# Performance work log

Hardware: AMD Instinct MI355X
Metric: run time of the kernel (lower is better)

The kernel has to match this reference:

```python
import jax, jax.numpy as jnp
import numpy as np

GAMMA = 0.99
ETA = 0.1
PHI = 0.9
EPS_FLOOR_NEWTON = 1e-8
EPS_FLOOR_BETA = 1e-6
N_NEWTON = 20


def _epsilon_cosh(r):
    # r: [B, N] nonnegative residuals; per-row Newton solve for epsilon s.t.
    # mean(sinh(r/eps)) == 1 along axis 1.
    N = r.shape[1]
    r_max = jnp.maximum(jnp.max(r, axis=1, keepdims=True), EPS_FLOOR_NEWTON)
    eps = r_max / (jnp.log(jnp.asarray(2.0 * N, dtype=r.dtype)) + EPS_FLOOR_NEWTON)
    for _ in range(N_NEWTON):
        eps_safe = jnp.maximum(eps, EPS_FLOOR_NEWTON)
        u = r / eps_safe  # [B, N]
        val = jnp.mean(jnp.sinh(u), axis=1, keepdims=True) - 1.0
        grad = jnp.mean(jnp.cosh(u) * (-u / eps_safe), axis=1, keepdims=True)
        eps = eps - val / (grad - EPS_FLOOR_NEWTON)
    return jnp.maximum(eps, EPS_FLOOR_NEWTON)


def _update_spatial_weights(r_i, Lambda, it):
    # 'cosh' weighting potential branch of update_spatial_weights
    del it  # unused by the cosh branch
    eps_q = _epsilon_cosh(r_i)                       # [B, 1]
    beta = 1.0 / (eps_q + EPS_FLOOR_BETA)            # [B, 1]
    q = jnp.sinh(beta * r_i)                         # [B, N]
    q_max = jnp.max(q, axis=1, keepdims=True)
    q_norm = q / (q_max + 1e-20)
    lambda_it = PHI * q_norm + (1.0 - PHI)
    return GAMMA * Lambda + ETA * lambda_it


def setup_inputs() -> dict:
    key = jax.random.key(0)
    k1, k2, k3 = jax.random.split(key, 3)
    B, N = 2048, 8192
    y_pred = jax.random.normal(k1, (B, N), dtype=jnp.float32)
    y_true = jax.random.normal(k2, (B, N), dtype=jnp.float32)
    Lambda = jax.random.uniform(k3, (B, N), dtype=jnp.float32)
    return {"y_pred": y_pred, "y_true": y_true, "Lambda": Lambda, "it": 100}


def reference(y_pred, y_true, Lambda, it):
    r_i = jnp.abs(y_true - y_pred)
    # weights are computed on detached residuals
    updated_Lambda = _update_spatial_weights(jax.lax.stop_gradient(r_i), Lambda, it)
    loss = jnp.mean(jnp.square(updated_Lambda * r_i))
    return (loss, updated_Lambda)
```

## Files before the change

### kernel.cpp

```cpp
#include <hip/hip_runtime.h>
#include <math.h>

#define N_COLS 8192
#define BLOCK  256
#define NW     4
#define F4PT   (N_COLS / BLOCK / 4)
#define NBINS  1024
#define BPL    (NBINS / 64)

__global__ void zero_out_kernel(float* out) {
    if (threadIdx.x == 0 && blockIdx.x == 0) out[0] = 0.0f;
}

__global__ __launch_bounds__(BLOCK) void custom_loss_kernel(
        const float* __restrict__ y_pred,
        const float* __restrict__ y_true,
        const float* __restrict__ Lambda,
        float* __restrict__ out,
        float inv_total) {
    __shared__ unsigned int s_hist[NBINS];
    __shared__ float s_wmax[NW];
    __shared__ float s_part[NW];
    __shared__ float s_bcast[2];

    const int row  = blockIdx.x;
    const int tid  = threadIdx.x;
    const int lane = tid & 63;
    const int wid  = tid >> 6;
    const size_t base = (size_t)row * N_COLS;
    const float4* yp4 = (const float4*)(y_pred + base);
    const float4* yt4 = (const float4*)(y_true + base);

    float4 r[F4PT];
    float rmax = 0.0f;
    #pragma unroll
    for (int j = 0; j < F4PT; ++j) {
        const int g = j * BLOCK + tid;
        float4 a = yt4[g];
        float4 b = yp4[g];
        float4 rv;
        rv.x = fabsf(a.x - b.x); rv.y = fabsf(a.y - b.y);
        rv.z = fabsf(a.z - b.z); rv.w = fabsf(a.w - b.w);
        r[j] = rv;
        rmax = fmaxf(rmax, fmaxf(fmaxf(rv.x, rv.y), fmaxf(rv.z, rv.w)));
    }
    #pragma unroll
    for (int m = 32; m >= 1; m >>= 1) rmax = fmaxf(rmax, __shfl_xor(rmax, m, 64));
    if (lane == 0) s_wmax[wid] = rmax;
    #pragma unroll
    for (int i = 0; i < NBINS / BLOCK; ++i) s_hist[tid + i * BLOCK] = 0u;
    __syncthreads();
    rmax = fmaxf(fmaxf(s_wmax[0], s_wmax[1]), fmaxf(s_wmax[2], s_wmax[3]));
    rmax = fmaxf(rmax, 1e-8f);

    const float hscale = (float)NBINS / rmax;
    #pragma unroll
    for (int j = 0; j < F4PT; ++j) {
        unsigned bx = min((unsigned)(r[j].x * hscale), (unsigned)(NBINS - 1));
        unsigned by = min((unsigned)(r[j].y * hscale), (unsigned)(NBINS - 1));
        unsigned bz = min((unsigned)(r[j].z * hscale), (unsigned)(NBINS - 1));
        unsigned bw = min((unsigned)(r[j].w * hscale), (unsigned)(NBINS - 1));
        atomicAdd(&s_hist[bx], 1u);
        atomicAdd(&s_hist[by], 1u);
        atomicAdd(&s_hist[bz], 1u);
        atomicAdd(&s_hist[bw], 1u);
    }
    __syncthreads();

    const float4* lam4 = (const float4*)(Lambda + base);
    float4 lam[F4PT];
    #pragma unroll
    for (int j = 0; j < F4PT; ++j) lam[j] = lam4[j * BLOCK + tid];

    if (wid == 0) {
        float eps = rmax / (logf(2.0f * (float)N_COLS) + 1e-8f);
        const float binw = rmax * (1.0f / (float)NBINS);
        const float sc2  = 0.5f / (float)N_COLS;
        for (int it = 0; it < 20; ++it) {
            const float inv_eps = __builtin_amdgcn_rcpf(fmaxf(eps, 1e-8f));
            const float d   = binw * inv_eps;
            const float d64 = 64.0f * d;
            float u  = ((float)lane + 0.5f) * d;
            float e  = __expf(u);
            float ei = __expf(-u);
            const float E  = __expf(d64);
            const float Ei = __expf(-d64);
            float fs = 0.0f, gs = 0.0f;
            #pragma unroll
            for (int k = 0; k < BPL; ++k) {
                const float n = (float)s_hist[lane + 64 * k];
                fs = fmaf(n, e - ei, fs);
                gs = fmaf(n * (e + ei), u, gs);
                e *= E; ei *= Ei; u += d64;
            }
            #pragma unroll
            for (int m2 = 32; m2 >= 1; m2 >>= 1) {
                fs += __shfl_xor(fs, m2, 64);
                gs += __shfl_xor(gs, m2, 64);
            }
            float val  = fmaf(fs, sc2, -1.0f);
            float grad = -(gs * sc2) * inv_eps;
            float delta = val * __builtin_amdgcn_rcpf(grad - 1e-8f);
            eps -= delta;
            if (fabsf(delta) <= 1e-5f * eps) break;
        }
        eps = fmaxf(eps, 1e-8f);
        const float beta = 1.0f / (eps + 1e-6f);
        const float um = beta * rmax;
        const float qmax = 0.5f * (__expf(um) - __expf(-um));
        if (lane == 0) {
            s_bcast[0] = beta;
            s_bcast[1] = 1.0f / (qmax + 1e-20f);
        }
    }
    __syncthreads();
    const float beta     = s_bcast[0];
    const float inv_qmax = s_bcast[1];

    float* outw = out + 1 + base;
    float s_loss = 0.0f;
    #pragma unroll
    for (int j = 0; j < F4PT; ++j) {
        const int g = j * BLOCK + tid;
        float rr[4] = {r[j].x, r[j].y, r[j].z, r[j].w};
        float LL[4] = {lam[j].x, lam[j].y, lam[j].z, lam[j].w};
        #pragma unroll
        for (int c = 0; c < 4; ++c) {
            float u  = beta * rr[c];
            float q  = 0.5f * (__expf(u) - __expf(-u));
            float lam_it = fmaf(0.9f, q * inv_qmax, 0.1f);
            float uL = fmaf(0.99f, LL[c], 0.1f * lam_it);
            outw[(size_t)g * 4 + c] = uL;
            float t = uL * rr[c];
            s_loss = fmaf(t, t, s_loss);
        }
    }
    #pragma unroll
    for (int m = 32; m >= 1; m >>= 1) s_loss += __shfl_xor(s_loss, m, 64);
    if (lane == 0) s_part[wid] = s_loss;
    __syncthreads();
    if (tid == 0) {
        float tot = (s_part[0] + s_part[1]) + (s_part[2] + s_part[3]);
        atomicAdd(out, tot * inv_total);
    }
}

extern "C" void kernel_launch(void* const* d_in, const int* in_sizes, int n_in,
                              void* d_out, int out_size, void* d_ws, size_t ws_size,
                              hipStream_t stream) {
    const float* y_pred = (const float*)d_in[0];
    const float* y_true = (const float*)d_in[1];
    const float* Lambda = (const float*)d_in[2];
    float* out = (float*)d_out;

    const int total = in_sizes[0];
    const int B = total / N_COLS;
    const float inv_total = 1.0f / (float)total;

    hipLaunchKernelGGL(zero_out_kernel, dim3(1), dim3(64), 0, stream, out);
    hipLaunchKernelGGL(custom_loss_kernel, dim3(B), dim3(BLOCK), 0, stream,
                       y_pred, y_true, Lambda, out, inv_total);
}
```

Baseline: 223.5 us.

## Split fused loss kernel into stats pass and epilogue pass

Splits the single per-row kernel into a stats kernel (max, histogram, Newton solve writing beta and inverse qmax to workspace) and an epilogue kernel that rereads y_pred and y_true, loads Lambda, and writes the updated weights and loss. The aim is to lower register pressure and raise occupancy, since the fused kernel kept residuals and Lambda in registers across the serial single-wave Newton loop. The cost is a second read of both inputs (about 134 MB extra traffic), which may partly come from L2/MALL, plus an extra kernel launch.

```diff
diff --git a/kernel.cpp b/kernel.cpp
--- a/kernel.cpp
+++ b/kernel.cpp
@@ -12,16 +12,12 @@
     if (threadIdx.x == 0 && blockIdx.x == 0) out[0] = 0.0f;
 }
 
-__global__ __launch_bounds__(BLOCK) void custom_loss_kernel(
+__global__ __launch_bounds__(BLOCK) void stats_kernel(
         const float* __restrict__ y_pred,
         const float* __restrict__ y_true,
-        const float* __restrict__ Lambda,
-        float* __restrict__ out,
-        float inv_total) {
+        float* __restrict__ ws) {
     __shared__ unsigned int s_hist[NBINS];
     __shared__ float s_wmax[NW];
-    __shared__ float s_part[NW];
-    __shared__ float s_bcast[2];
 
     const int row  = blockIdx.x;
     const int tid  = threadIdx.x;
@@ -67,11 +63,6 @@
     }
     __syncthreads();
 
-    const float4* lam4 = (const float4*)(Lambda + base);
-    float4 lam[F4PT];
-    #pragma unroll
-    for (int j = 0; j < F4PT; ++j) lam[j] = lam4[j * BLOCK + tid];
-
     if (wid == 0) {
         float eps = rmax / (logf(2.0f * (float)N_COLS) + 1e-8f);
         const float binw = rmax * (1.0f / (float)NBINS);
@@ -109,21 +100,52 @@
         const float um = beta * rmax;
         const float qmax = 0.5f * (__expf(um) - __expf(-um));
         if (lane == 0) {
-            s_bcast[0] = beta;
-            s_bcast[1] = 1.0f / (qmax + 1e-20f);
+            ws[2 * row]     = beta;
+            ws[2 * row + 1] = 1.0f / (qmax + 1e-20f);
         }
     }
-    __syncthreads();
-    const float beta     = s_bcast[0];
-    const float inv_qmax = s_bcast[1];
+}
+
+__global__ __launch_bounds__(BLOCK) void epilogue_kernel(
+        const float* __restrict__ y_pred,
+        const float* __restrict__ y_true,
+        const float* __restrict__ Lambda,
+        const float* __restrict__ ws,
+        float* __restrict__ out,
+        float inv_total) {
+    __shared__ float s_part[NW];
+
+    const int row  = blockIdx.x;
+    const int tid  = threadIdx.x;
+    const int lane = tid & 63;
+    const int wid  = tid >> 6;
+    const size_t base = (size_t)row * N_COLS;
+    const float4* yp4 = (const float4*)(y_pred + base);
+    const float4* yt4 = (const float4*)(y_true + base);
+    const float4* lam4 = (const float4*)(Lambda + base);
+    const float beta     = ws[2 * row];
+    const float inv_qmax = ws[2 * row + 1];
+
+    float4 r[F4PT];
+    #pragma unroll
+    for (int j = 0; j < F4PT; ++j) {
+        const int g = j * BLOCK + tid;
+        float4 a = yt4[g];
+        float4 b = yp4[g];
+        float4 rv;
+        rv.x = fabsf(a.x - b.x); rv.y = fabsf(a.y - b.y);
+        rv.z = fabsf(a.z - b.z); rv.w = fabsf(a.w - b.w);
+        r[j] = rv;
+    }
 
     float* outw = out + 1 + base;
     float s_loss = 0.0f;
     #pragma unroll
     for (int j = 0; j < F4PT; ++j) {
         const int g = j * BLOCK + tid;
+        float4 L = lam4[g];
         float rr[4] = {r[j].x, r[j].y, r[j].z, r[j].w};
-        float LL[4] = {lam[j].x, lam[j].y, lam[j].z, lam[j].w};
+        float LL[4] = {L.x, L.y, L.z, L.w};
         #pragma unroll
         for (int c = 0; c < 4; ++c) {
             float u  = beta * rr[c];
@@ -152,12 +174,15 @@
     const float* y_true = (const float*)d_in[1];
     const float* Lambda = (const float*)d_in[2];
     float* out = (float*)d_out;
+    float* ws  = (float*)d_ws;
 
     const int total = in_sizes[0];
     const int B = total / N_COLS;
     const float inv_total = 1.0f / (float)total;
 
     hipLaunchKernelGGL(zero_out_kernel, dim3(1), dim3(64), 0, stream, out);
-    hipLaunchKernelGGL(custom_loss_kernel, dim3(B), dim3(BLOCK), 0, stream,
-                       y_pred, y_true, Lambda, out, inv_total);
+    hipLaunchKernelGGL(stats_kernel, dim3(B), dim3(BLOCK), 0, stream,
+                       y_pred, y_true, ws);
+    hipLaunchKernelGGL(epilogue_kernel, dim3(B), dim3(BLOCK), 0, stream,
+                       y_pred, y_true, Lambda, ws, out, inv_total);
 }
```

Measured after the change: 234.9 us. 1.05x slower.

## Realign Lambda output stores to 16 bytes via lane shuffles and per-wave chunks

Applied to the files above, without the earlier changes.

The output weights start one float past the buffer base, so the earlier per-element stores were not 16-byte aligned. Each wave now owns a contiguous quarter of the row and computes all its updated weights first. It then shifts them by three floats with cross-lane shuffles, so most stores become aligned float4 writes, and a few scalar writes cover the head and tail. The Newton loop also keeps the histogram counts in registers and replaces the xor-shuffle reductions with DPP-based wave sums. The cost is extra shuffles and more live registers for the staged outputs.

```diff
diff --git a/kernel.cpp b/kernel.cpp
--- a/kernel.cpp
+++ b/kernel.cpp
@@ -4,12 +4,26 @@
 #define N_COLS 8192
 #define BLOCK  256
 #define NW     4
-#define F4PT   (N_COLS / BLOCK / 4)
+#define CHUNK  (N_COLS / NW)
+#define KG     (CHUNK / 256)
 #define NBINS  1024
 #define BPL    (NBINS / 64)
 
 __global__ void zero_out_kernel(float* out) {
     if (threadIdx.x == 0 && blockIdx.x == 0) out[0] = 0.0f;
+}
+
+__device__ __forceinline__ float wave64_sum_dpp(float x) {
+    union fi { float f; int i; };
+    fi v, t; v.f = x;
+    t.i = __builtin_amdgcn_update_dpp(0, v.i, 0x111, 0xf, 0xf, true); v.f += t.f;
+    t.i = __builtin_amdgcn_update_dpp(0, v.i, 0x112, 0xf, 0xf, true); v.f += t.f;
+    t.i = __builtin_amdgcn_update_dpp(0, v.i, 0x114, 0xf, 0xf, true); v.f += t.f;
+    t.i = __builtin_amdgcn_update_dpp(0, v.i, 0x118, 0xf, 0xf, true); v.f += t.f;
+    t.i = __builtin_amdgcn_update_dpp(0, v.i, 0x142, 0xa, 0xf, true); v.f += t.f;
+    t.i = __builtin_amdgcn_update_dpp(0, v.i, 0x143, 0xc, 0xf, true); v.f += t.f;
+    v.i = __builtin_amdgcn_readlane(v.i, 63);
+    return v.f;
 }
 
 __global__ __launch_bounds__(BLOCK) void custom_loss_kernel(
@@ -28,20 +42,21 @@
     const int lane = tid & 63;
     const int wid  = tid >> 6;
     const size_t base = (size_t)row * N_COLS;
+    const int f4base = wid * (CHUNK / 4) + lane;
     const float4* yp4 = (const float4*)(y_pred + base);
     const float4* yt4 = (const float4*)(y_true + base);
 
-    float4 r[F4PT];
+    float4 r[KG];
     float rmax = 0.0f;
     #pragma unroll
-    for (int j = 0; j < F4PT; ++j) {
-        const int g = j * BLOCK + tid;
+    for (int k = 0; k < KG; ++k) {
+        const int g = f4base + k * 64;
         float4 a = yt4[g];
         float4 b = yp4[g];
         float4 rv;
         rv.x = fabsf(a.x - b.x); rv.y = fabsf(a.y - b.y);
         rv.z = fabsf(a.z - b.z); rv.w = fabsf(a.w - b.w);
-        r[j] = rv;
+        r[k] = rv;
         rmax = fmaxf(rmax, fmaxf(fmaxf(rv.x, rv.y), fmaxf(rv.z, rv.w)));
     }
     #pragma unroll
@@ -55,11 +70,11 @@
 
     const float hscale = (float)NBINS / rmax;
     #pragma unroll
-    for (int j = 0; j < F4PT; ++j) {
-        unsigned bx = min((unsigned)(r[j].x * hscale), (unsigned)(NBINS - 1));
-        unsigned by = min((unsigned)(r[j].y * hscale), (unsigned)(NBINS - 1));
-        unsigned bz = min((unsigned)(r[j].z * hscale), (unsigned)(NBINS - 1));
-        unsigned bw = min((unsigned)(r[j].w * hscale), (unsigned)(NBINS - 1));
+    for (int k = 0; k < KG; ++k) {
+        unsigned bx = min((unsigned)(r[k].x * hscale), (unsigned)(NBINS - 1));
+        unsigned by = min((unsigned)(r[k].y * hscale), (unsigned)(NBINS - 1));
+        unsigned bz = min((unsigned)(r[k].z * hscale), (unsigned)(NBINS - 1));
+        unsigned bw = min((unsigned)(r[k].w * hscale), (unsigned)(NBINS - 1));
         atomicAdd(&s_hist[bx], 1u);
         atomicAdd(&s_hist[by], 1u);
         atomicAdd(&s_hist[bz], 1u);
@@ -68,11 +83,15 @@
     __syncthreads();
 
     const float4* lam4 = (const float4*)(Lambda + base);
-    float4 lam[F4PT];
-    #pragma unroll
-    for (int j = 0; j < F4PT; ++j) lam[j] = lam4[j * BLOCK + tid];
+    float4 lam[KG];
+    #pragma unroll
+    for (int k = 0; k < KG; ++k) lam[k] = lam4[f4base + k * 64];
 
     if (wid == 0) {
+        float nreg[BPL];
+        #pragma unroll
+        for (int k = 0; k < BPL; ++k) nreg[k] = (float)s_hist[lane + 64 * k];
+
         float eps = rmax / (logf(2.0f * (float)N_COLS) + 1e-8f);
         const float binw = rmax * (1.0f / (float)NBINS);
         const float sc2  = 0.5f / (float)N_COLS;
@@ -88,16 +107,13 @@
             float fs = 0.0f, gs = 0.0f;
             #pragma unroll
             for (int k = 0; k < BPL; ++k) {
-                const float n = (float)s_hist[lane + 64 * k];
+                const float n = nreg[k];
                 fs = fmaf(n, e - ei, fs);
                 gs = fmaf(n * (e + ei), u, gs);
                 e *= E; ei *= Ei; u += d64;
             }
-            #pragma unroll
-            for (int m2 = 32; m2 >= 1; m2 >>= 1) {
-                fs += __shfl_xor(fs, m2, 64);
-                gs += __shfl_xor(gs, m2, 64);
-            }
+            fs = wave64_sum_dpp(fs);
+            gs = wave64_sum_dpp(gs);
             float val  = fmaf(fs, sc2, -1.0f);
             float grad = -(gs * sc2) * inv_eps;
             float delta = val * __builtin_amdgcn_rcpf(grad - 1e-8f);
@@ -117,24 +133,47 @@
     const float beta     = s_bcast[0];
     const float inv_qmax = s_bcast[1];
 
-    float* outw = out + 1 + base;
+    float4 uL[KG];
     float s_loss = 0.0f;
-    #pragma unroll
-    for (int j = 0; j < F4PT; ++j) {
-        const int g = j * BLOCK + tid;
-        float rr[4] = {r[j].x, r[j].y, r[j].z, r[j].w};
-        float LL[4] = {lam[j].x, lam[j].y, lam[j].z, lam[j].w};
-        #pragma unroll
-        for (int c = 0; c < 4; ++c) {
-            float u  = beta * rr[c];
-            float q  = 0.5f * (__expf(u) - __expf(-u));
-            float lam_it = fmaf(0.9f, q * inv_qmax, 0.1f);
-            float uL = fmaf(0.99f, LL[c], 0.1f * lam_it);
-            outw[(size_t)g * 4 + c] = uL;
-            float t = uL * rr[c];
-            s_loss = fmaf(t, t, s_loss);
+    #define EMA1(RR, LL, DST) { \
+        float u_ = beta * (RR); \
+        float q_ = 0.5f * (__expf(u_) - __expf(-u_)); \
+        float li_ = fmaf(0.9f, q_ * inv_qmax, 0.1f);    \
+        (DST) = fmaf(0.99f, (LL), 0.1f * li_);          \
+        float t_ = (DST) * (RR); \
+        s_loss = fmaf(t_, t_, s_loss); }
+    #pragma unroll
+    for (int k = 0; k < KG; ++k) {
+        EMA1(r[k].x, lam[k].x, uL[k].x);
+        EMA1(r[k].y, lam[k].y, uL[k].y);
+        EMA1(r[k].z, lam[k].z, uL[k].z);
+        EMA1(r[k].w, lam[k].w, uL[k].w);
+    }
+    #undef EMA1
+
+    float* outw = out + 1 + base + (size_t)wid * CHUNK;
+    const int src = (lane + 1) & 63;
+    #pragma unroll
+    for (int k = 0; k < KG; ++k) {
+        const float4 cur = uL[k];
+        const float4 nxt = uL[(k + 1) & (KG - 1)];
+        float sx = (lane == 0) ? nxt.x : cur.x;
+        float sy = (lane == 0) ? nxt.y : cur.y;
+        float sz = (lane == 0) ? nxt.z : cur.z;
+        float4 vv;
+        vv.x = cur.w;
+        vv.y = __shfl(sx, src, 64);
+        vv.z = __shfl(sy, src, 64);
+        vv.w = __shfl(sz, src, 64);
+        if (!(k == KG - 1 && lane == 63)) {
+            *(float4*)(outw + k * 256 + lane * 4 + 3) = vv;
         }
     }
+    if (lane == 0) {
+        outw[0] = uL[0].x; outw[1] = uL[0].y; outw[2] = uL[0].z;
+    }
+    if (lane == 63) outw[CHUNK - 1] = uL[KG - 1].w;
+
     #pragma unroll
     for (int m = 32; m >= 1; m >>= 1) s_loss += __shfl_xor(s_loss, m, 64);
     if (lane == 0) s_part[wid] = s_loss;
```

Result: no change. 225.6 us (+0.9%).
